# Kernel tuning notes

Hardware: AMD Instinct MI355X
Metric: run time of the kernel (lower is better)

Reference implementation:

```python
import jax, jax.numpy as jnp
import numpy as np

# Static config matching init_kwargs
NUM_EXPERTS = 8
CAP_FACTOR = 1.0
MIN_CAP = 8


def setup_inputs() -> dict:
    key = jax.random.key(0)
    ks = jax.random.split(key, 10)
    G, S, D, H, E = 4, 4096, 1024, 4096, NUM_EXPERTS
    s = 0.02  # init stddev like nn.initializers.normal(0.02)
    return {
        "x": jax.random.normal(ks[0], (G, S, D), dtype=jnp.float32),
        "gate": jax.random.normal(ks[1], (D, E), dtype=jnp.float32) * s,
        "W1": jax.random.normal(ks[2], (E, D, H), dtype=jnp.float32) * s,
        "b1": jnp.zeros((E, H), dtype=jnp.float32),
        "W2": jax.random.normal(ks[3], (E, H, D), dtype=jnp.float32) * s,
        "b2": jnp.zeros((E, D), dtype=jnp.float32),
        "Ws1": jax.random.normal(ks[4], (D, H), dtype=jnp.float32) * s,
        "bs1": jnp.zeros((H,), dtype=jnp.float32),
        "Ws2": jax.random.normal(ks[5], (H, D), dtype=jnp.float32) * s,
        "bs2": jnp.zeros((D,), dtype=jnp.float32),
    }


def reference(x, gate, W1, b1, W2, b2, Ws1, bs1, Ws2, bs2):
    G, S, D = x.shape
    E = gate.shape[1]
    T = G * S
    capacity = max(MIN_CAP, int(CAP_FACTOR * T / E))  # static -> 2048

    # ---- Router (inference path: indices + scores, loss = 0) ----
    logits = jnp.einsum('gsd,de->gse', x, gate)           # (G,S,E)
    probs = jax.nn.softmax(logits, axis=-1)
    flat_probs = probs.transpose(2, 0, 1).reshape(E, T)    # (E,T)
    # capacity <= T here, so padding width is 0 (kept implicit)
    scores, token_idx = jax.lax.top_k(flat_probs, k=capacity)  # (E,C)
    scores = jnp.where(scores > -1e8, scores, 0.0)

    # ---- Routed experts: gather -> per-expert FFN (grouped GEMM) -> scatter-add
    flat_x = x.reshape(T, D)
    tok = flat_x[token_idx]                                # (E,C,D) gather
    h = jax.nn.gelu(jnp.einsum('ecd,edh->ech', tok, W1) + b1[:, None, :])
    out_tok = jnp.einsum('ech,ehd->ecd', h, W2) + b2[:, None, :]
    scaled = out_tok * scores[..., None]                   # weight by routing prob
    routed = jnp.zeros_like(flat_x).at[token_idx.reshape(-1)].add(
        scaled.reshape(E * capacity, D)).reshape(G, S, D)

    # ---- Shared expert (single FFN applied to all tokens) ----
    shared = jax.nn.gelu(jnp.einsum('gsd,dh->gsh', x, Ws1) + bs1)
    shared = jnp.einsum('gsh,hd->gsd', shared, Ws2) + bs2

    return routed + shared
```

## Files before the change

kernel.cpp:

```cpp
#include <hip/hip_runtime.h>
#include <hip/hip_bf16.h>

using bf16 = __hip_bfloat16;
typedef short v8s __attribute__((ext_vector_type(8)));
typedef float v4f __attribute__((ext_vector_type(4)));
typedef int v4i __attribute__((ext_vector_type(4)));

#define NE 8
#define NT 16384
#define ND 1024
#define NH 4096
#define CAP 2048

__device__ __forceinline__ void load_lds16(const void* g, void* s) {
  __builtin_amdgcn_global_load_lds(
      (const __attribute__((address_space(1))) unsigned int*)g,
      (__attribute__((address_space(3))) unsigned int*)s, 16, 0, 0);
}

__device__ __forceinline__ float gelu_tanh(float x) {
  float u = 0.7978845608028654f * (x + 0.044715f * x * x * x);
  float e = __expf(2.0f * u);
  float t = 1.0f - 2.0f / (e + 1.0f);
  return 0.5f * x * (1.0f + t);
}

__global__ __launch_bounds__(256) void tcvt64(const float* __restrict__ src,
                                              bf16* __restrict__ dst, int R, int C) {
  __shared__ float tile[128][65];
  size_t mo = (size_t)blockIdx.z * R * C;
  int c0 = blockIdx.x * 64, r0 = blockIdx.y * 128;
  int lane = threadIdx.x & 63, wv = threadIdx.x >> 6;
  for (int i = wv; i < 128; i += 4)
    tile[i][lane] = src[mo + (size_t)(r0 + i) * C + c0 + lane];
  __syncthreads();
  for (int j = wv; j < 64; j += 4) {
    bf16 o0 = __float2bfloat16(tile[2 * lane][j]);
    bf16 o1 = __float2bfloat16(tile[2 * lane + 1][j]);
    ushort2 pk = make_ushort2(*(unsigned short*)&o0, *(unsigned short*)&o1);
    *(ushort2*)((unsigned short*)dst + mo + (size_t)(c0 + j) * R + r0 + 2 * lane) = pk;
  }
}

__global__ __launch_bounds__(256) void colmax_k(const float* __restrict__ src,
                                                float* __restrict__ sc, int R, int C) {
  size_t mo = (size_t)blockIdx.y * R * C;
  int c = blockIdx.x * 256 + threadIdx.x;
  const float* p = src + mo + c;
  float m = 1e-30f;
#pragma unroll 8
  for (int r = 0; r < R; r++) m = fmaxf(m, fabsf(p[(size_t)r * C]));
  sc[(size_t)blockIdx.y * C + c] = m * (1.0f / 127.0f);
}

__global__ __launch_bounds__(256) void tq_k(const float* __restrict__ src,
                                            const float* __restrict__ scl,
                                            signed char* __restrict__ dst, int R, int C) {
  __shared__ float tile[128][65];
  size_t mo = (size_t)blockIdx.z * R * C;
  size_t so = (size_t)blockIdx.z * C;
  int c0 = blockIdx.x * 64, r0 = blockIdx.y * 128;
  int lane = threadIdx.x & 63, wv = threadIdx.x >> 6;
  for (int i = wv; i < 128; i += 4)
    tile[i][lane] = src[mo + (size_t)(r0 + i) * C + c0 + lane];
  __syncthreads();
  for (int j = wv; j < 64; j += 4) {
    float inv = 1.0f / scl[so + c0 + j];
    int b0 = (int)rintf(tile[2 * lane][j] * inv);
    int b1 = (int)rintf(tile[2 * lane + 1][j] * inv);
    unsigned short pk = (unsigned short)((b0 & 255) | ((b1 & 255) << 8));
    *(unsigned short*)(dst + mo + (size_t)(c0 + j) * R + r0 + 2 * lane) = pk;
  }
}

__global__ __launch_bounds__(256) void rowq_f(const float* __restrict__ in,
                                              signed char* __restrict__ q,
                                              float* __restrict__ sc,
                                              int L, int nrows) {
  int row = blockIdx.x * 4 + (threadIdx.x >> 6);
  if (row >= nrows) return;
  int lane = threadIdx.x & 63;
  const int epl = L >> 6;
  const float* src = in + (size_t)row * L + lane * epl;
  float m = 1e-30f;
  for (int i = 0; i < epl; i += 4) {
    float4 v = *(const float4*)(src + i);
    m = fmaxf(m, fmaxf(fmaxf(fabsf(v.x), fabsf(v.y)), fmaxf(fabsf(v.z), fabsf(v.w))));
  }
#pragma unroll
  for (int off = 32; off > 0; off >>= 1) m = fmaxf(m, __shfl_xor(m, off));
  float inv = 127.0f / m;
  signed char* dq = q + (size_t)row * L + lane * epl;
  for (int i = 0; i < epl; i += 4) {
    float4 v = *(const float4*)(src + i);
    int b0 = (int)rintf(v.x * inv), b1 = (int)rintf(v.y * inv);
    int b2 = (int)rintf(v.z * inv), b3 = (int)rintf(v.w * inv);
    unsigned pk = (unsigned)(b0 & 255) | ((unsigned)(b1 & 255) << 8) |
                  ((unsigned)(b2 & 255) << 16) | ((unsigned)(b3 & 255) << 24);
    *(unsigned*)(dq + i) = pk;
  }
  if (lane == 0) sc[row] = m * (1.0f / 127.0f);
}

__global__ __launch_bounds__(256) void router_k(const float* __restrict__ x,
                                                const float* __restrict__ gate,
                                                float* __restrict__ probs) {
  int wave = threadIdx.x >> 6, lane = threadIdx.x & 63;
  int t = blockIdx.x * 4 + wave;
  const float* xr = x + (size_t)t * ND;
  double acc[NE];
#pragma unroll
  for (int e = 0; e < NE; e++) acc[e] = 0.0;
  for (int d = lane; d < ND; d += 64) {
    double xv = (double)xr[d];
    const float* g = gate + d * NE;
#pragma unroll
    for (int e = 0; e < NE; e++) acc[e] += xv * (double)g[e];
  }
#pragma unroll
  for (int e = 0; e < NE; e++) {
    double v = acc[e];
#pragma unroll
    for (int off = 32; off > 0; off >>= 1) v += __shfl_xor(v, off);
    acc[e] = v;
  }
  if (lane == 0) {
    float l[NE], m = -1e30f;
#pragma unroll
    for (int e = 0; e < NE; e++) { l[e] = (float)acc[e]; m = fmaxf(m, l[e]); }
    float p[NE], s = 0.f;
#pragma unroll
    for (int e = 0; e < NE; e++) { p[e] = expf(l[e] - m); s += p[e]; }
#pragma unroll
    for (int e = 0; e < NE; e++) probs[e * NT + t] = p[e] / s;
  }
}

__global__ __launch_bounds__(1024) void topk_k(const float* __restrict__ probs,
                                               unsigned* __restrict__ thr_key,
                                               int* __restrict__ needed,
                                               int* __restrict__ cnt) {
  int e = blockIdx.x;
  const float* p = probs + e * NT;
  __shared__ int hist[256];
  __shared__ unsigned s_pref;
  __shared__ int s_rank;
  unsigned prefix = 0;
  int rank = CAP;
  for (int rd = 0; rd < 4; rd++) {
    int shift = 24 - rd * 8;
    if (threadIdx.x < 256) hist[threadIdx.x] = 0;
    __syncthreads();
    unsigned mask = (rd == 0) ? 0u : (0xFFFFFFFFu << (shift + 8));
    for (int t = threadIdx.x; t < NT; t += 1024) {
      unsigned k = __float_as_uint(p[t]);
      if ((k & mask) == prefix) atomicAdd(&hist[(k >> shift) & 255], 1);
    }
    __syncthreads();
    if (threadIdx.x == 0) {
      int cum = 0, b = 255;
      for (;;) {
        int c = hist[b];
        if (cum + c >= rank || b == 0) break;
        cum += c; b--;
      }
      s_pref = prefix | ((unsigned)b << shift);
      s_rank = rank - cum;
    }
    __syncthreads();
    prefix = s_pref; rank = s_rank;
    __syncthreads();
  }
  if (threadIdx.x == 0) {
    thr_key[e] = prefix; needed[e] = rank;
    cnt[e] = 0; cnt[NE + e] = 0;
  }
}

__global__ __launch_bounds__(256) void compact_k(const float* __restrict__ probs,
                                                 const unsigned* __restrict__ thr_key,
                                                 const int* __restrict__ needed,
                                                 int* __restrict__ cnt, int* __restrict__ eqc,
                                                 int* __restrict__ tok, float* __restrict__ scr) {
  int gid = blockIdx.x * 256 + threadIdx.x;
  int e = gid >> 14, t = gid & (NT - 1);
  float pv = probs[gid];
  unsigned k = __float_as_uint(pv);
  unsigned thr = thr_key[e];
  int nd = needed[e];
  bool gt = k > thr, eq = k == thr;
  unsigned long long mgt = __ballot(gt), meq = __ballot(eq);
  int lane = threadIdx.x & 63, wv = threadIdx.x >> 6;
  __shared__ int wcnt[2][4];
  __shared__ int base[2];
  if (lane == 0) { wcnt[0][wv] = __popcll(mgt); wcnt[1][wv] = __popcll(meq); }
  __syncthreads();
  if (threadIdx.x == 0) {
    int s0 = wcnt[0][0] + wcnt[0][1] + wcnt[0][2] + wcnt[0][3];
    int s1 = wcnt[1][0] + wcnt[1][1] + wcnt[1][2] + wcnt[1][3];
    base[0] = s0 ? atomicAdd(&cnt[e], s0) : 0;
    base[1] = s1 ? atomicAdd(&eqc[e], s1) : 0;
  }
  __syncthreads();
  unsigned long long lm = (1ull << lane) - 1ull;
  if (gt) {
    int p = __popcll(mgt & lm);
    for (int w = 0; w < wv; w++) p += wcnt[0][w];
    int slot = base[0] + p;
    tok[e * CAP + slot] = t; scr[e * CAP + slot] = pv;
  } else if (eq) {
    int q = base[1] + __popcll(meq & lm);
    for (int w = 0; w < wv; w++) q += wcnt[1][w];
    if (q < nd) {
      int slot = (CAP - nd) + q;
      tok[e * CAP + slot] = t; scr[e * CAP + slot] = pv;
    }
  }
}

#define BAR() __builtin_amdgcn_s_barrier()
#define SBAR0() __builtin_amdgcn_sched_barrier(0)

#define XCD_SWZ(m0, n0)                                                       \
  const int hw_ = blockIdx.y * gridDim.x + blockIdx.x;                        \
  const int ntx_ = gridDim.x;                                                 \
  const int chunk_ = gridDim.y >> 3;                                          \
  const int xcd_ = hw_ & 7;                                                   \
  const int i2_ = hw_ >> 3;                                                   \
  const int lm_ = i2_ / ntx_;                                                 \
  const int ln_ = i2_ - lm_ * ntx_;                                           \
  const int m0 = (xcd_ * chunk_ + lm_) << 8;                                  \
  const int n0 = ln_ << 8;

template <int MODE>
__global__ __launch_bounds__(512, 2) void gemm256(
    const bf16* __restrict__ A, int lda, const int* __restrict__ rowmap,
    const bf16* __restrict__ BT, long long bstride, int gshift,
    const float* __restrict__ bias, int bias_stride,
    int N, int K,
    bf16* __restrict__ outH, float* __restrict__ outF,
    const int* __restrict__ tok, const float* __restrict__ scr) {
  __shared__ __attribute__((aligned(16))) char lds[131072];
  const int tid = threadIdx.x;
  const int lane = tid & 63, wv = tid >> 6;
  const int wr = wv >> 2, wc = wv & 3;
  XCD_SWZ(m0, n0);
  const int grp = m0 >> gshift;
  const bf16* Bp = BT + (size_t)grp * (size_t)bstride;
  const float* bp = bias + (size_t)grp * (size_t)bias_stride;
  const int nt = K >> 6;

  const int srow = tid >> 3;
  const int gc = (tid & 7) ^ (srow & 7);
  const bf16* srcA[4]; const bf16* srcB[4];
#pragma unroll
  for (int g = 0; g < 4; g++) {
    int am = m0 + g * 64 + srow;
    int ar = rowmap ? rowmap[am] : am;
    srcA[g] = A + (size_t)ar * lda + gc * 8;
    srcB[g] = Bp + (size_t)(n0 + g * 64 + srow) * K + gc * 8;
  }
  auto stageA = [&](int t, int h) {
    char* d = lds + ((t & 1) * 65536 + h * 16384) + tid * 16;
    load_lds16(srcA[h * 2 + 0] + (size_t)t * 64, d);
    load_lds16(srcA[h * 2 + 1] + (size_t)t * 64, d + 8192);
  };
  auto stageB = [&](int t, int h) {
    char* d = lds + ((t & 1) * 65536 + 32768 + h * 16384) + tid * 16;
    load_lds16(srcB[h * 2 + 0] + (size_t)t * 64, d);
    load_lds16(srcB[h * 2 + 1] + (size_t)t * 64, d + 8192);
  };

  const int fr = lane & 15, hi = lane >> 4;
  const int xr = fr & 7;
  const int cb0 = ((0 + hi) ^ xr) << 4;
  const int cb1 = ((4 + hi) ^ xr) << 4;
  const int arow = ((wr << 7) + fr) << 7;
  const int brow = ((wc << 6) + fr) << 7;

  v4f acc[8][4] = {};
  v8s a03[4][2], a47[4][2], b01[2][2], b23[2][2];

#define R_A03(BASE)                                                           \
  _Pragma("unroll") for (int mi = 0; mi < 4; mi++) {                          \
    a03[mi][0] = *(const v8s*)((BASE) + arow + mi * 2048 + cb0);              \
    a03[mi][1] = *(const v8s*)((BASE) + arow + mi * 2048 + cb1);              \
  }
#define R_A47(BASE)                                                           \
  _Pragma("unroll") for (int mi = 0; mi < 4; mi++) {                          \
    a47[mi][0] = *(const v8s*)((BASE) + arow + (4 + mi) * 2048 + cb0);        \
    a47[mi][1] = *(const v8s*)((BASE) + arow + (4 + mi) * 2048 + cb1);        \
  }
#define R_B01(BASE)                                                           \
  _Pragma("unroll") for (int ni = 0; ni < 2; ni++) {                          \
    b01[ni][0] = *(const v8s*)((BASE) + brow + ni * 2048 + cb0);              \
    b01[ni][1] = *(const v8s*)((BASE) + brow + ni * 2048 + cb1);              \
  }
#define R_B23(BASE)                                                           \
  _Pragma("unroll") for (int ni = 0; ni < 2; ni++) {                          \
    b23[ni][0] = *(const v8s*)((BASE) + brow + (2 + ni) * 2048 + cb0);        \
    b23[ni][1] = *(const v8s*)((BASE) + brow + (2 + ni) * 2048 + cb1);        \
  }
#define MFMA_Q(AB, BB, MOFF, NOFF)                                            \
  __builtin_amdgcn_s_setprio(1);                                              \
  _Pragma("unroll") for (int kk = 0; kk < 2; kk++)                            \
  _Pragma("unroll") for (int mi = 0; mi < 4; mi++)                            \
  _Pragma("unroll") for (int ni = 0; ni < 2; ni++)                            \
    acc[(MOFF) + mi][(NOFF) + ni] = __builtin_amdgcn_mfma_f32_16x16x32_bf16(  \
        AB[mi][kk], BB[ni][kk], acc[(MOFF) + mi][(NOFF) + ni], 0, 0, 0);      \
  __builtin_amdgcn_s_setprio(0);

  stageA(0, 0); stageA(0, 1); stageB(0, 0); stageB(0, 1);
  if (nt > 1) { stageB(1, 0); stageB(1, 1); }
  if (nt > 1) { asm volatile("s_waitcnt vmcnt(4)" ::: "memory"); }
  else        { asm volatile("s_waitcnt vmcnt(0)" ::: "memory"); }
  BAR();
  {
    const char* Ab0 = lds; const char* Bb0 = lds + 32768;
    R_A03(Ab0); R_B01(Bb0); R_B23(Bb0); R_A47(Ab0);
  }

  for (int t = 0; t < nt; ++t) {
    const char* AbN = lds + ((t + 1) & 1) * 65536;
    const char* BbN = AbN + 32768;
    asm volatile("s_waitcnt lgkmcnt(12)" ::: "memory"); SBAR0();
    MFMA_Q(a03, b01, 0, 0);
    if (t + 1 < nt) stageA(t + 1, 0);
    asm volatile("s_waitcnt lgkmcnt(8)" ::: "memory"); SBAR0();
    MFMA_Q(a03, b23, 0, 2);
    if (t + 1 < nt) stageA(t + 1, 1);
    BAR();
    asm volatile("s_waitcnt lgkmcnt(0)" ::: "memory"); SBAR0();
    MFMA_Q(a47, b01, 4, 0);
    if (t + 2 < nt) stageB(t + 2, 0);
    if (t + 2 < nt) stageB(t + 2, 1);
    if (t + 2 < nt) { asm volatile("s_waitcnt vmcnt(4)" ::: "memory"); }
    else            { asm volatile("s_waitcnt vmcnt(0)" ::: "memory"); }
    BAR();
    if (t + 1 < nt) { R_A03(AbN); R_B01(BbN); }
    MFMA_Q(a47, b23, 4, 2);
    if (t + 1 < nt) { R_B23(BbN); R_A47(AbN); }
  }
  asm volatile("s_waitcnt vmcnt(0) lgkmcnt(0)" ::: "memory");

  float bv[4];
#pragma unroll
  for (int ni = 0; ni < 4; ni++) bv[ni] = bp[n0 + (wc << 6) + ni * 16 + fr];
  const int rbase = m0 + (wr << 7) + (hi << 2);
#pragma unroll
  for (int mi = 0; mi < 8; mi++) {
#pragma unroll
    for (int r = 0; r < 4; r++) {
      int gm = rbase + mi * 16 + r;
      int trow = 0; float sv = 0.f;
      if (MODE == 2) { trow = tok[gm]; sv = scr[gm]; }
#pragma unroll
      for (int ni = 0; ni < 4; ni++) {
        int gn = n0 + (wc << 6) + ni * 16 + fr;
        float v = acc[mi][ni][r] + bv[ni];
        if (MODE == 0)      outH[(size_t)gm * N + gn] = __float2bfloat16(gelu_tanh(v));
        else if (MODE == 1) outF[(size_t)gm * N + gn] = v;
        else                atomicAdd(outF + (size_t)trow * N + gn, v * sv);
      }
    }
  }
}

__global__ __launch_bounds__(512, 2) void gemm256q(
    const signed char* __restrict__ A, int K, const int* __restrict__ rowmap,
    const signed char* __restrict__ BT, long long bstride, int gshift,
    const float* __restrict__ sxr, const float* __restrict__ swc, int sw_stride,
    const float* __restrict__ bias, int bias_stride, int N,
    bf16* __restrict__ outH) {
  __shared__ __attribute__((aligned(16))) char lds[131072];
  const int tid = threadIdx.x;
  const int lane = tid & 63, wv = tid >> 6;
  const int wr = wv >> 2, wc = wv & 3;
  XCD_SWZ(m0, n0);
  const int grp = m0 >> gshift;
  const signed char* Bp = BT + (size_t)grp * (size_t)bstride;
  const float* bp = bias + (size_t)grp * (size_t)bias_stride;
  const float* swp = swc + (size_t)grp * (size_t)sw_stride;
  const int nt = K >> 7;

  const int srow = tid >> 3;
  const int gc = (tid & 7) ^ (srow & 7);
  const signed char* srcA[4]; const signed char* srcB[4];
#pragma unroll
  for (int g = 0; g < 4; g++) {
    int am = m0 + g * 64 + srow;
    int ar = rowmap ? rowmap[am] : am;
    srcA[g] = A + (size_t)ar * K + gc * 16;
    srcB[g] = Bp + (size_t)(n0 + g * 64 + srow) * K + gc * 16;
  }
  auto stageA = [&](int t, int h) {
    char* d = lds + ((t & 1) * 65536 + h * 16384) + tid * 16;
    load_lds16(srcA[h * 2 + 0] + (size_t)t * 128, d);
    load_lds16(srcA[h * 2 + 1] + (size_t)t * 128, d + 8192);
  };
  auto stageB = [&](int t, int h) {
    char* d = lds + ((t & 1) * 65536 + 32768 + h * 16384) + tid * 16;
    load_lds16(srcB[h * 2 + 0] + (size_t)t * 128, d);
    load_lds16(srcB[h * 2 + 1] + (size_t)t * 128, d + 8192);
  };

  const int fr = lane & 15, hi = lane >> 4;
  const int xr = fr & 7;
  const int cb0 = ((0 + hi) ^ xr) << 4;
  const int cb1 = ((4 + hi) ^ xr) << 4;
  const int arow = ((wr << 7) + fr) << 7;
  const int brow = ((wc << 6) + fr) << 7;

  v4i acc[8][4] = {};
  v4i a03[4][2], a47[4][2], b01[2][2], b23[2][2];

#define QR_A03(BASE)                                                          \
  _Pragma("unroll") for (int mi = 0; mi < 4; mi++) {                          \
    a03[mi][0] = *(const v4i*)((BASE) + arow + mi * 2048 + cb0);              \
    a03[mi][1] = *(const v4i*)((BASE) + arow + mi * 2048 + cb1);              \
  }
#define QR_A47(BASE)                                                          \
  _Pragma("unroll") for (int mi = 0; mi < 4; mi++) {                          \
    a47[mi][0] = *(const v4i*)((BASE) + arow + (4 + mi) * 2048 + cb0);        \
    a47[mi][1] = *(const v4i*)((BASE) + arow + (4 + mi) * 2048 + cb1);        \
  }
#define QR_B01(BASE)                                                          \
  _Pragma("unroll") for (int ni = 0; ni < 2; ni++) {                          \
    b01[ni][0] = *(const v4i*)((BASE) + brow + ni * 2048 + cb0);              \
    b01[ni][1] = *(const v4i*)((BASE) + brow + ni * 2048 + cb1);              \
  }
#define QR_B23(BASE)                                                          \
  _Pragma("unroll") for (int ni = 0; ni < 2; ni++) {                          \
    b23[ni][0] = *(const v4i*)((BASE) + brow + (2 + ni) * 2048 + cb0);        \
    b23[ni][1] = *(const v4i*)((BASE) + brow + (2 + ni) * 2048 + cb1);        \
  }
#define QMFMA_Q(AB, BB, MOFF, NOFF)                                           \
  __builtin_amdgcn_s_setprio(1);                                              \
  _Pragma("unroll") for (int kk = 0; kk < 2; kk++)                            \
  _Pragma("unroll") for (int mi = 0; mi < 4; mi++)                            \
  _Pragma("unroll") for (int ni = 0; ni < 2; ni++)                            \
    acc[(MOFF) + mi][(NOFF) + ni] = __builtin_amdgcn_mfma_i32_16x16x64_i8(    \
        AB[mi][kk], BB[ni][kk], acc[(MOFF) + mi][(NOFF) + ni], 0, 0, 0);      \
  __builtin_amdgcn_s_setprio(0);

  stageA(0, 0); stageA(0, 1); stageB(0, 0); stageB(0, 1);
  stageB(1, 0); stageB(1, 1);
  asm volatile("s_waitcnt vmcnt(4)" ::: "memory");
  BAR();
  {
    const char* Ab0 = lds; const char* Bb0 = lds + 32768;
    QR_A03(Ab0); QR_B01(Bb0); QR_B23(Bb0); QR_A47(Ab0);
  }

  for (int t = 0; t < nt; ++t) {
    const char* AbN = lds + ((t + 1) & 1) * 65536;
    const char* BbN = AbN + 32768;
    asm volatile("s_waitcnt lgkmcnt(12)" ::: "memory"); SBAR0();
    QMFMA_Q(a03, b01, 0, 0);
    if (t + 1 < nt) stageA(t + 1, 0);
    asm volatile("s_waitcnt lgkmcnt(8)" ::: "memory"); SBAR0();
    QMFMA_Q(a03, b23, 0, 2);
    if (t + 1 < nt) stageA(t + 1, 1);
    BAR();
    asm volatile("s_waitcnt lgkmcnt(0)" ::: "memory"); SBAR0();
    QMFMA_Q(a47, b01, 4, 0);
    if (t + 2 < nt) stageB(t + 2, 0);
    if (t + 2 < nt) stageB(t + 2, 1);
    if (t + 2 < nt) { asm volatile("s_waitcnt vmcnt(4)" ::: "memory"); }
    else            { asm volatile("s_waitcnt vmcnt(0)" ::: "memory"); }
    BAR();
    if (t + 1 < nt) { QR_A03(AbN); QR_B01(BbN); }
    QMFMA_Q(a47, b23, 4, 2);
    if (t + 1 < nt) { QR_B23(BbN); QR_A47(AbN); }
  }
  asm volatile("s_waitcnt vmcnt(0) lgkmcnt(0)" ::: "memory");

  float bv[4], swv[4];
#pragma unroll
  for (int ni = 0; ni < 4; ni++) {
    int gn = n0 + (wc << 6) + ni * 16 + fr;
    bv[ni] = bp[gn]; swv[ni] = swp[gn];
  }
  const int rbase = m0 + (wr << 7) + (hi << 2);
#pragma unroll
  for (int mi = 0; mi < 8; mi++) {
#pragma unroll
    for (int r = 0; r < 4; r++) {
      int gm = rbase + mi * 16 + r;
      float sxa = sxr[rowmap ? rowmap[gm] : gm];
#pragma unroll
      for (int ni = 0; ni < 4; ni++) {
        int gn = n0 + (wc << 6) + ni * 16 + fr;
        float v = (float)acc[mi][ni][r] * (sxa * swv[ni]) + bv[ni];
        outH[(size_t)gm * N + gn] = __float2bfloat16(gelu_tanh(v));
      }
    }
  }
}

extern "C" void kernel_launch(void* const* d_in, const int* in_sizes, int n_in,
                              void* d_out, int out_size, void* d_ws, size_t ws_size,
                              hipStream_t stream) {
  const float* x   = (const float*)d_in[0];
  const float* gate= (const float*)d_in[1];
  const float* W1  = (const float*)d_in[2];
  const float* b1  = (const float*)d_in[3];
  const float* W2  = (const float*)d_in[4];
  const float* b2  = (const float*)d_in[5];
  const float* Ws1 = (const float*)d_in[6];
  const float* bs1 = (const float*)d_in[7];
  const float* Ws2 = (const float*)d_in[8];
  const float* bs2 = (const float*)d_in[9];
  float* out = (float*)d_out;

  char* w = (char*)d_ws;
  size_t off = 0;
  auto alloc = [&](size_t bytes) {
    void* p = w + off;
    off = (off + bytes + 255) & ~(size_t)255;
    return p;
  };
  bf16* w2T   = (bf16*)alloc((size_t)NE * ND * NH * 2);
  bf16* ws2T  = (bf16*)alloc((size_t)ND * NH * 2);
  bf16* h     = (bf16*)alloc((size_t)NT * NH * 2);
  signed char* xq   = (signed char*)alloc((size_t)NT * ND);
  signed char* w1q  = (signed char*)alloc((size_t)NE * NH * ND);
  signed char* ws1q = (signed char*)alloc((size_t)NH * ND);
  float* sx   = (float*)alloc((size_t)NT * 4);
  float* sw1  = (float*)alloc((size_t)NE * NH * 4);
  float* sws1 = (float*)alloc((size_t)NH * 4);
  float* probs= (float*)alloc((size_t)NE * NT * 4);
  unsigned* thr = (unsigned*)alloc(NE * 4);
  int* needed = (int*)alloc(NE * 4);
  int* cnt    = (int*)alloc(2 * NE * 4);
  int* eqc    = cnt + NE;
  int* tok    = (int*)alloc((size_t)NE * CAP * 4);
  float* scr  = (float*)alloc((size_t)NE * CAP * 4);
  (void)alloc(65536);
  if (off > ws_size) return;

  tcvt64<<<dim3(ND / 64, NH / 128, NE), 256, 0, stream>>>(W2, w2T, NH, ND);
  tcvt64<<<dim3(ND / 64, NH / 128, 1), 256, 0, stream>>>(Ws2, ws2T, NH, ND);
  colmax_k<<<dim3(NH / 256, NE), 256, 0, stream>>>(W1, sw1, ND, NH);
  colmax_k<<<dim3(NH / 256, 1), 256, 0, stream>>>(Ws1, sws1, ND, NH);
  tq_k<<<dim3(NH / 64, ND / 128, NE), 256, 0, stream>>>(W1, sw1, w1q, ND, NH);
  tq_k<<<dim3(NH / 64, ND / 128, 1), 256, 0, stream>>>(Ws1, sws1, ws1q, ND, NH);
  rowq_f<<<NT / 4, 256, 0, stream>>>(x, xq, sx, ND, NT);

  router_k<<<NT / 4, 256, 0, stream>>>(x, gate, probs);
  topk_k<<<NE, 1024, 0, stream>>>(probs, thr, needed, cnt);
  compact_k<<<NE * NT / 256, 256, 0, stream>>>(probs, thr, needed, cnt, eqc, tok, scr);

  gemm256q<<<dim3(NH / 256, NT / 256), 512, 0, stream>>>(
      xq, ND, nullptr, ws1q, 0, 30, sx, sws1, 0, bs1, 0, NH, h);
  gemm256<1><<<dim3(ND / 256, NT / 256), 512, 0, stream>>>(
      h, NH, nullptr, ws2T, 0, 30, bs2, 0, ND, NH, nullptr, out, nullptr, nullptr);

  gemm256q<<<dim3(NH / 256, NT / 256), 512, 0, stream>>>(
      xq, ND, tok, w1q, (long long)NH * ND, 11, sx, sw1, NH, b1, NH, NH, h);
  gemm256<2><<<dim3(ND / 256, NT / 256), 512, 0, stream>>>(
      h, NH, nullptr, w2T, (long long)ND * NH, 11, b2, ND, ND, NH, nullptr, out, tok, scr);
}
```

Before: 899.6 us.

## Merge shared and routed int8 up-projections into one launch; parallelize weight colmax

The shared and routed int8 first-layer GEMMs now run as one launch with a z dimension of 2, each writing to its own hidden buffer. This doubles the grid per launch, removing the tail of two separate launches and letting the two GEMMs overlap. Column-max scaling is split across row chunks that combine through an atomicMax on float bits, after a zeroing kernel. Row quantization of x is fused with the router so x is read once. The cost is a second full-size hidden buffer and some extra atomics.

```diff
diff --git a/kernel.cpp b/kernel.cpp
--- a/kernel.cpp
+++ b/kernel.cpp
@@ -23,6 +23,11 @@
   float e = __expf(2.0f * u);
   float t = 1.0f - 2.0f / (e + 1.0f);
   return 0.5f * x * (1.0f + t);
+}
+
+__global__ __launch_bounds__(256) void zf(unsigned* p, int n) {
+  int i = blockIdx.x * 256 + threadIdx.x;
+  if (i < n) p[i] = 0;
 }
 
 __global__ __launch_bounds__(256) void tcvt64(const float* __restrict__ src,
@@ -42,15 +47,17 @@
   }
 }
 
-__global__ __launch_bounds__(256) void colmax_k(const float* __restrict__ src,
-                                                float* __restrict__ sc, int R, int C) {
-  size_t mo = (size_t)blockIdx.y * R * C;
+__global__ __launch_bounds__(256) void colmax_par(const float* __restrict__ src,
+                                                  unsigned* __restrict__ scm,
+                                                  int R, int C) {
+  size_t mo = (size_t)blockIdx.z * R * C;
   int c = blockIdx.x * 256 + threadIdx.x;
-  const float* p = src + mo + c;
-  float m = 1e-30f;
+  int r0 = blockIdx.y * 128;
+  const float* p = src + mo + (size_t)r0 * C + c;
+  float m = 0.f;
 #pragma unroll 8
-  for (int r = 0; r < R; r++) m = fmaxf(m, fabsf(p[(size_t)r * C]));
-  sc[(size_t)blockIdx.y * C + c] = m * (1.0f / 127.0f);
+  for (int r = 0; r < 128; r++) m = fmaxf(m, fabsf(p[(size_t)r * C]));
+  atomicMax(scm + (size_t)blockIdx.z * C + c, __float_as_uint(m));
 }
 
 __global__ __launch_bounds__(256) void tq_k(const float* __restrict__ src,
@@ -65,7 +72,7 @@
     tile[i][lane] = src[mo + (size_t)(r0 + i) * C + c0 + lane];
   __syncthreads();
   for (int j = wv; j < 64; j += 4) {
-    float inv = 1.0f / scl[so + c0 + j];
+    float inv = 127.0f / fmaxf(scl[so + c0 + j], 1e-30f);
     int b0 = (int)rintf(tile[2 * lane][j] * inv);
     int b1 = (int)rintf(tile[2 * lane + 1][j] * inv);
     unsigned short pk = (unsigned short)((b0 & 255) | ((b1 & 255) << 8));
@@ -73,66 +80,61 @@
   }
 }
 
-__global__ __launch_bounds__(256) void rowq_f(const float* __restrict__ in,
-                                              signed char* __restrict__ q,
-                                              float* __restrict__ sc,
-                                              int L, int nrows) {
+__global__ __launch_bounds__(256) void xprep_k(const float* __restrict__ x,
+                                               const float* __restrict__ gate,
+                                               signed char* __restrict__ xq,
+                                               float* __restrict__ sx,
+                                               float* __restrict__ probs) {
   int row = blockIdx.x * 4 + (threadIdx.x >> 6);
-  if (row >= nrows) return;
   int lane = threadIdx.x & 63;
-  const int epl = L >> 6;
-  const float* src = in + (size_t)row * L + lane * epl;
+  const float* src = x + (size_t)row * ND + lane * 16;
+  float v[16];
+  *(float4*)(v + 0)  = *(const float4*)(src + 0);
+  *(float4*)(v + 4)  = *(const float4*)(src + 4);
+  *(float4*)(v + 8)  = *(const float4*)(src + 8);
+  *(float4*)(v + 12) = *(const float4*)(src + 12);
   float m = 1e-30f;
-  for (int i = 0; i < epl; i += 4) {
-    float4 v = *(const float4*)(src + i);
-    m = fmaxf(m, fmaxf(fmaxf(fabsf(v.x), fabsf(v.y)), fmaxf(fabsf(v.z), fabsf(v.w))));
-  }
+#pragma unroll
+  for (int i = 0; i < 16; i++) m = fmaxf(m, fabsf(v[i]));
 #pragma unroll
   for (int off = 32; off > 0; off >>= 1) m = fmaxf(m, __shfl_xor(m, off));
   float inv = 127.0f / m;
-  signed char* dq = q + (size_t)row * L + lane * epl;
-  for (int i = 0; i < epl; i += 4) {
-    float4 v = *(const float4*)(src + i);
-    int b0 = (int)rintf(v.x * inv), b1 = (int)rintf(v.y * inv);
-    int b2 = (int)rintf(v.z * inv), b3 = (int)rintf(v.w * inv);
-    unsigned pk = (unsigned)(b0 & 255) | ((unsigned)(b1 & 255) << 8) |
-                  ((unsigned)(b2 & 255) << 16) | ((unsigned)(b3 & 255) << 24);
-    *(unsigned*)(dq + i) = pk;
-  }
-  if (lane == 0) sc[row] = m * (1.0f / 127.0f);
-}
-
-__global__ __launch_bounds__(256) void router_k(const float* __restrict__ x,
-                                                const float* __restrict__ gate,
-                                                float* __restrict__ probs) {
-  int wave = threadIdx.x >> 6, lane = threadIdx.x & 63;
-  int t = blockIdx.x * 4 + wave;
-  const float* xr = x + (size_t)t * ND;
+  unsigned pk[4];
+#pragma unroll
+  for (int j = 0; j < 4; j++) {
+    int b0 = (int)rintf(v[j * 4 + 0] * inv), b1 = (int)rintf(v[j * 4 + 1] * inv);
+    int b2 = (int)rintf(v[j * 4 + 2] * inv), b3 = (int)rintf(v[j * 4 + 3] * inv);
+    pk[j] = (unsigned)(b0 & 255) | ((unsigned)(b1 & 255) << 8) |
+            ((unsigned)(b2 & 255) << 16) | ((unsigned)(b3 & 255) << 24);
+  }
+  *(uint4*)(xq + (size_t)row * ND + lane * 16) = make_uint4(pk[0], pk[1], pk[2], pk[3]);
+  if (lane == 0) sx[row] = m * (1.0f / 127.0f);
   double acc[NE];
 #pragma unroll
   for (int e = 0; e < NE; e++) acc[e] = 0.0;
-  for (int d = lane; d < ND; d += 64) {
-    double xv = (double)xr[d];
-    const float* g = gate + d * NE;
-#pragma unroll
-    for (int e = 0; e < NE; e++) acc[e] += xv * (double)g[e];
+  const float* g = gate + (size_t)(lane * 16) * NE;
+#pragma unroll 4
+  for (int i = 0; i < 16; i++) {
+    double xv = (double)v[i];
+#pragma unroll
+    for (int e = 0; e < NE; e++) acc[e] += xv * (double)g[i * NE + e];
   }
 #pragma unroll
   for (int e = 0; e < NE; e++) {
-    double v = acc[e];
-#pragma unroll
-    for (int off = 32; off > 0; off >>= 1) v += __shfl_xor(v, off);
-    acc[e] = v;
+    double t = acc[e];
+#pragma unroll
+    for (int off = 32; off > 0; off >>= 1) t += __shfl_xor(t, off);
+    acc[e] = t;
   }
   if (lane == 0) {
-    float l[NE], m = -1e30f;
-#pragma unroll
-    for (int e = 0; e < NE; e++) { l[e] = (float)acc[e]; m = fmaxf(m, l[e]); }
+    float l[NE], mx = -1e30f;
+#pragma unroll
+    for (int e = 0; e < NE; e++) { l[e] = (float)acc[e]; mx = fmaxf(mx, l[e]); }
     float p[NE], s = 0.f;
 #pragma unroll
-    for (int e = 0; e < NE; e++) { p[e] = expf(l[e] - m); s += p[e]; }
-#pragma unroll
-    for (int e = 0; e < NE; e++) probs[e * NT + t] = p[e] / s;
+    for (int e = 0; e < NE; e++) { p[e] = expf(l[e] - mx); s += p[e]; }
+#pragma unroll
+    for (int e = 0; e < NE; e++) probs[e * NT + row] = p[e] / s;
   }
 }
 
@@ -367,20 +369,26 @@
 }
 
 __global__ __launch_bounds__(512, 2) void gemm256q(
-    const signed char* __restrict__ A, int K, const int* __restrict__ rowmap,
-    const signed char* __restrict__ BT, long long bstride, int gshift,
-    const float* __restrict__ sxr, const float* __restrict__ swc, int sw_stride,
-    const float* __restrict__ bias, int bias_stride, int N,
-    bf16* __restrict__ outH) {
+    const signed char* __restrict__ A,
+    const int* __restrict__ tok,
+    const signed char* __restrict__ Bsh, const signed char* __restrict__ Brt,
+    const float* __restrict__ sxr,
+    const float* __restrict__ swsh, const float* __restrict__ swrt,
+    const float* __restrict__ bsh, const float* __restrict__ brt,
+    bf16* __restrict__ hsh, bf16* __restrict__ hrt) {
   __shared__ __attribute__((aligned(16))) char lds[131072];
+  const int K = ND, N = NH;
+  const bool routed = blockIdx.z != 0;
   const int tid = threadIdx.x;
   const int lane = tid & 63, wv = tid >> 6;
   const int wr = wv >> 2, wc = wv & 3;
   XCD_SWZ(m0, n0);
-  const int grp = m0 >> gshift;
-  const signed char* Bp = BT + (size_t)grp * (size_t)bstride;
-  const float* bp = bias + (size_t)grp * (size_t)bias_stride;
-  const float* swp = swc + (size_t)grp * (size_t)sw_stride;
+  const int grp = routed ? (m0 >> 11) : 0;
+  const int* rowmap = routed ? tok : nullptr;
+  const signed char* Bp = routed ? (Brt + (size_t)grp * ((size_t)NH * ND)) : Bsh;
+  const float* bp = routed ? (brt + grp * NH) : bsh;
+  const float* swp = routed ? (swrt + grp * NH) : swsh;
+  bf16* outH = routed ? hrt : hsh;
   const int nt = K >> 7;
 
   const int srow = tid >> 3;
@@ -479,7 +487,7 @@
 #pragma unroll
   for (int ni = 0; ni < 4; ni++) {
     int gn = n0 + (wc << 6) + ni * 16 + fr;
-    bv[ni] = bp[gn]; swv[ni] = swp[gn];
+    bv[ni] = bp[gn]; swv[ni] = swp[gn] * (1.0f / 127.0f);
   }
   const int rbase = m0 + (wr << 7) + (hi << 2);
 #pragma unroll
@@ -522,14 +530,16 @@
   };
   bf16* w2T   = (bf16*)alloc((size_t)NE * ND * NH * 2);
   bf16* ws2T  = (bf16*)alloc((size_t)ND * NH * 2);
-  bf16* h     = (bf16*)alloc((size_t)NT * NH * 2);
+  bf16* hs    = (bf16*)alloc((size_t)NT * NH * 2);
+  bf16* hr    = (bf16*)alloc((size_t)NT * NH * 2);
   signed char* xq   = (signed char*)alloc((size_t)NT * ND);
   signed char* w1q  = (signed char*)alloc((size_t)NE * NH * ND);
   signed char* ws1q = (signed char*)alloc((size_t)NH * ND);
-  float* sx   = (float*)alloc((size_t)NT * 4);
-  float* sw1  = (float*)alloc((size_t)NE * NH * 4);
-  float* sws1 = (float*)alloc((size_t)NH * 4);
-  float* probs= (float*)alloc((size_t)NE * NT * 4);
+  float* sx    = (float*)alloc((size_t)NT * 4);
+  float* swmax = (float*)alloc((size_t)(NE + 1) * NH * 4);
+  float* sw1   = swmax;
+  float* sws1  = swmax + (size_t)NE * NH;
+  float* probs = (float*)alloc((size_t)NE * NT * 4);
   unsigned* thr = (unsigned*)alloc(NE * 4);
   int* needed = (int*)alloc(NE * 4);
   int* cnt    = (int*)alloc(2 * NE * 4);
@@ -539,25 +549,23 @@
   (void)alloc(65536);
   if (off > ws_size) return;
 
+  zf<<<((NE + 1) * NH + 255) / 256, 256, 0, stream>>>((unsigned*)swmax, (NE + 1) * NH);
   tcvt64<<<dim3(ND / 64, NH / 128, NE), 256, 0, stream>>>(W2, w2T, NH, ND);
   tcvt64<<<dim3(ND / 64, NH / 128, 1), 256, 0, stream>>>(Ws2, ws2T, NH, ND);
-  colmax_k<<<dim3(NH / 256, NE), 256, 0, stream>>>(W1, sw1, ND, NH);
-  colmax_k<<<dim3(NH / 256, 1), 256, 0, stream>>>(Ws1, sws1, ND, NH);
+  colmax_par<<<dim3(NH / 256, ND / 128, NE), 256, 0, stream>>>(W1, (unsigned*)sw1, ND, NH);
+  colmax_par<<<dim3(NH / 256, ND / 128, 1), 256, 0, stream>>>(Ws1, (unsigned*)sws1, ND, NH);
   tq_k<<<dim3(NH / 64, ND / 128, NE), 256, 0, stream>>>(W1, sw1, w1q, ND, NH);
   tq_k<<<dim3(NH / 64, ND / 128, 1), 256, 0, stream>>>(Ws1, sws1, ws1q, ND, NH);
-  rowq_f<<<NT / 4, 256, 0, stream>>>(x, xq, sx, ND, NT);
-
-  router_k<<<NT / 4, 256, 0, stream>>>(x, gate, probs);
+
+  xprep_k<<<NT / 4, 256, 0, stream>>>(x, gate, xq, sx, probs);
   topk_k<<<NE, 1024, 0, stream>>>(probs, thr, needed, cnt);
   compact_k<<<NE * NT / 256, 256, 0, stream>>>(probs, thr, needed, cnt, eqc, tok, scr);
 
-  gemm256q<<<dim3(NH / 256, NT / 256), 512, 0, stream>>>(
-      xq, ND, nullptr, ws1q, 0, 30, sx, sws1, 0, bs1, 0, NH, h);
+  gemm256q<<<dim3(NH / 256, NT / 256, 2), 512, 0, stream>>>(
+      xq, tok, ws1q, w1q, sx, sws1, sw1, bs1, b1, hs, hr);
+
   gemm256<1><<<dim3(ND / 256, NT / 256), 512, 0, stream>>>(
-      h, NH, nullptr, ws2T, 0, 30, bs2, 0, ND, NH, nullptr, out, nullptr, nullptr);
-
-  gemm256q<<<dim3(NH / 256, NT / 256), 512, 0, stream>>>(
-      xq, ND, tok, w1q, (long long)NH * ND, 11, sx, sw1, NH, b1, NH, NH, h);
+      hs, NH, nullptr, ws2T, 0, 30, bs2, 0, ND, NH, nullptr, out, nullptr, nullptr);
   gemm256<2><<<dim3(ND / 256, NT / 256), 512, 0, stream>>>(
-      h, NH, nullptr, w2T, (long long)ND * NH, 11, b2, ND, ND, NH, nullptr, out, tok, scr);
-}
+      hr, NH, nullptr, w2T, (long long)ND * NH, 11, b2, ND, ND, NH, nullptr, out, tok, scr);
+}
```

Result: faster. 865.7 us (-3.8%).
